# Kernel tuning notes

Measured on AMD Instinct MI355X. Metric: run time of the kernel, lower is better.

## Reference

```python
import jax, jax.numpy as jnp
import numpy as np

NUM_HEADS = 32
HEAD_DIM = 64
ROPE_THETA = 10000.0


def _rope_cos_sin(position_ids, head_dim, theta):
    # inv_freq: [head_dim/2]
    half = head_dim // 2
    inv_freq = 1.0 / (theta ** (jnp.arange(0, half, dtype=jnp.float32) * 2.0 / head_dim))
    angles = position_ids.astype(jnp.float32)[..., None] * inv_freq  # [B,S,half]
    return jnp.cos(angles), jnp.sin(angles)


def _apply_rope(x, cos, sin):
    # x: [B,S,H,hd]; cos/sin: [B,S,half] -> broadcast over heads (rotate-half, Llama style)
    half = x.shape[-1] // 2
    x1, x2 = x[..., :half], x[..., half:]
    c = cos[:, :, None, :]
    s = sin[:, :, None, :]
    return jnp.concatenate([x1 * c - x2 * s, x2 * c + x1 * s], axis=-1)


def setup_inputs() -> dict:
    key = jax.random.key(0)
    ks = jax.random.split(key, 8)
    B, S, D = 2, 2048, 2048
    hidden_states = jax.random.normal(ks[0], (B, S, D), dtype=jnp.float32)
    # causal additive mask (is_causal=False in IpexSDP; mask carries causality)
    causal = jnp.tril(jnp.ones((S, S), dtype=jnp.bool_))
    attention_mask = jnp.where(causal, 0.0, -1e9).astype(jnp.float32)[None, None, :, :]
    attention_mask = jnp.broadcast_to(attention_mask, (B, 1, S, S))
    position_ids = jnp.broadcast_to(jnp.arange(S, dtype=jnp.int64)[None, :], (B, S))
    scale = 0.02
    qkv_w = jax.random.normal(ks[1], (3, D, D), dtype=jnp.float32) * scale
    qkv_b = jax.random.normal(ks[2], (3, D), dtype=jnp.float32) * scale
    o_w = jax.random.normal(ks[3], (D, D), dtype=jnp.float32) * scale
    o_b = jax.random.normal(ks[4], (D,), dtype=jnp.float32) * scale
    residual = jax.random.normal(ks[5], (B, S, D), dtype=jnp.float32)
    return {
        'hidden_states': hidden_states,
        'attention_mask': attention_mask,
        'position_ids': position_ids,
        'qkv_w': qkv_w,
        'qkv_b': qkv_b,
        'o_w': o_w,
        'o_b': o_b,
        'residual': residual,
    }


def reference(hidden_states, attention_mask, position_ids, qkv_w, qkv_b, o_w, o_b, residual):
    B, S, D = hidden_states.shape
    H, hd = NUM_HEADS, HEAD_DIM
    # fused QKV projection (weights stored transposed: x @ W), matching mm_qkv_out
    qkv = jnp.einsum('bsd,tde->tbse', hidden_states, qkv_w) + qkv_b[:, None, None, :]
    q = qkv[0].reshape(B, S, H, hd)
    k = qkv[1].reshape(B, S, H, hd)
    v = qkv[2].reshape(B, S, H, hd)
    cos, sin = _rope_cos_sin(position_ids, hd, ROPE_THETA)
    q = _apply_rope(q, cos, sin)
    k = _apply_rope(k, cos, sin)
    scale = 1.0 / jnp.sqrt(jnp.asarray(hd, dtype=hidden_states.dtype))
    # [B,H,S,S]
    scores = jnp.einsum('bqhd,bkhd->bhqk', q, k) * scale + attention_mask
    probs = jax.nn.softmax(scores, axis=-1)
    attn = jnp.einsum('bhqk,bkhd->bqhd', probs, v).reshape(B, S, D)
    # o-proj fused with bias + residual add (matmul_add_add)
    out = attn @ o_w + o_b + residual
    return out
```

## Files before the change

kernel.cpp:

```cpp
#include <hip/hip_runtime.h>
#include <stdint.h>
#include <stdio.h>

#define D_MODEL 2048
#define SEQ     2048
#define NHEADS  32
#define HDIM    64
#define BATCH   2
#define BH      (BATCH * NHEADS)
#define GK      2048

typedef unsigned short u16;
typedef unsigned int   u32;
typedef __attribute__((ext_vector_type(8))) short short8;
typedef __attribute__((ext_vector_type(4))) short s16x4;
typedef __attribute__((ext_vector_type(4))) float f32x4;
typedef __attribute__((ext_vector_type(4))) u32   u32x4;
typedef __attribute__((ext_vector_type(2))) u32   u32x2;

__device__ __forceinline__ float bf2f(u16 x) {
  union { u32 u; float f; } c; c.u = ((u32)x) << 16; return c.f;
}
__device__ __forceinline__ u16 f2bf(float f) {
  union { float f; u32 u; } c; c.f = f;
  u32 u = c.u;
  return (u16)((u + 0x7FFFu + ((u >> 16) & 1u)) >> 16);
}
__device__ __forceinline__ u32 fbits(float f) {
  union { float f; u32 u; } c; c.f = f; return c.u;
}

typedef const __attribute__((address_space(1))) u32* gas_t;
typedef __attribute__((address_space(3))) u32* las_t;
__device__ __forceinline__ void gll16(const void* g, void* l) {
  __builtin_amdgcn_global_load_lds((gas_t)g, (las_t)l, 16, 0, 0);
}

__device__ __forceinline__ void swiz_mn(int pid, int nx, int& mtile, int& ntile) {
  int chunk = 8 * nx;
  int grp = pid / chunk, loc = pid - grp * chunk;
  mtile = grp * 8 + (loc & 7);
  ntile = loc >> 3;
}

__global__ __launch_bounds__(256) void cvt_k(const float* __restrict__ in,
                                             u16* __restrict__ out) {
  int id = blockIdx.x * 256 + threadIdx.x;
  f32x4 v = *(const f32x4*)&in[(size_t)id * 4];
  alignas(8) u16 o[4];
#pragma unroll
  for (int j = 0; j < 4; j++) o[j] = f2bf(v[j]);
  *(u32x2*)&out[(size_t)id * 4] = *(const u32x2*)o;
}

__global__ __launch_bounds__(256) void transpose_cvt_k(const float* __restrict__ qkv_w,
                                                       const float* __restrict__ o_w,
                                                       u16* __restrict__ outT) {
  __shared__ u16 tile[64][72];
  const int z = blockIdx.z;
  const float* inz = (z < 3) ? qkv_w + (size_t)z * D_MODEL * D_MODEL : o_w;
  u16* outz = outT + (size_t)z * D_MODEL * D_MODEL;
  const int r0 = blockIdx.y * 64, c0 = blockIdx.x * 64;
  const int t = threadIdx.x;
  const int lrow = t >> 4, lcol4 = (t & 15) * 4;
#pragma unroll
  for (int i = 0; i < 4; i++) {
    int r = lrow + i * 16;
    f32x4 v = *(const f32x4*)&inz[(size_t)(r0 + r) * D_MODEL + (c0 + lcol4)];
#pragma unroll
    for (int j = 0; j < 4; j++) tile[r][lcol4 + j] = f2bf(v[j]);
  }
  __syncthreads();
  const int row = t >> 3, col8 = (t & 7) * 8;
#pragma unroll
  for (int i = 0; i < 2; i++) {
    int r = row + i * 32;
    alignas(16) u16 vals[8];
#pragma unroll
    for (int j = 0; j < 8; j++) vals[j] = tile[col8 + j][r];
    *(u32x4*)&outz[(size_t)(c0 + r) * D_MODEL + (r0 + col8)] = *(const u32x4*)vals;
  }
}

__device__ __forceinline__ void gemm128(const u16* __restrict__ A, const u16* __restrict__ BT,
                                        int m0, int n0, u16* As, u16* Bs, f32x4 acc[4][4]) {
  const int t = threadIdx.x;
  const int lane = t & 63, w = t >> 6;
  const int quad = lane >> 4, l16 = lane & 15;
  const int wr = w >> 1, wc = w & 1;
  const int ldr = lane >> 2, ldc = (lane & 3) * 8;
#pragma unroll
  for (int mt = 0; mt < 4; mt++)
#pragma unroll
    for (int nt = 0; nt < 4; nt++)
#pragma unroll
      for (int i = 0; i < 4; i++) acc[mt][nt][i] = 0.0f;

  for (int k0 = 0; k0 < GK; k0 += 32) {
    __syncthreads();
#pragma unroll
    for (int i = 0; i < 2; i++) {
      int rbase = w * 32 + i * 16;
      gll16(&A[(size_t)(m0 + rbase + ldr) * GK + k0 + ldc], &As[rbase * 32]);
      gll16(&BT[(size_t)(n0 + rbase + ldr) * GK + k0 + ldc], &Bs[rbase * 32]);
    }
    __syncthreads();
    short8 af[4], bf[4];
#pragma unroll
    for (int mt = 0; mt < 4; mt++)
      af[mt] = *(const short8*)&As[(wr * 64 + mt * 16 + l16) * 32 + quad * 8];
#pragma unroll
    for (int nt = 0; nt < 4; nt++)
      bf[nt] = *(const short8*)&Bs[(wc * 64 + nt * 16 + l16) * 32 + quad * 8];
#pragma unroll
    for (int mt = 0; mt < 4; mt++)
#pragma unroll
      for (int nt = 0; nt < 4; nt++)
        acc[mt][nt] = __builtin_amdgcn_mfma_f32_16x16x32_bf16(af[mt], bf[nt], acc[mt][nt], 0, 0, 0);
  }
}


__device__ __forceinline__ short8 lds_frag(const u16* tile, int row, int kh, int quad) {
  int off = row * 128 + ((kh * 64 + quad * 16) ^ ((row & 7) << 4));
  return *(const short8*)((const char*)tile + off);
}

__device__ __forceinline__ void stage_half(const u16* __restrict__ src, int rowbase, int k0,
                                           u16* tile, int h, int w, int srl, int scol) {
  u16* ldsb = tile + h * (128 * 64);
  const u16* g0 = &src[(size_t)(rowbase + h * 128 + srl) * GK + k0 + scol];
  const u16* g1 = &src[(size_t)(rowbase + h * 128 + srl + 8) * GK + k0 + scol];
  gll16(g0, (char*)ldsb + w * 2048);
  gll16(g1, (char*)ldsb + w * 2048 + 1024);
}

__global__ __launch_bounds__(512, 1) void qkv_gemm256_k(const u16* __restrict__ A,
                                                        const u16* __restrict__ BT,
                                                        const float* __restrict__ bias,
                                                        u16* __restrict__ Qb, u16* __restrict__ Kb,
                                                        u16* __restrict__ Vbt) {
  __shared__ u16 As[2][256 * 64];
  __shared__ u16 Bs[2][256 * 64];
  const int t = threadIdx.x, w = t >> 6, lane = t & 63;
  const int quad = lane >> 4, l16 = lane & 15;
  const int wr = w >> 2, wc = w & 3;
  int mtile, ntile;
  swiz_mn(blockIdx.x, 24, mtile, ntile);
  const int m0 = mtile * 256, n0 = ntile * 256;
  const int srl = w * 16 + (lane >> 3);
  const int scol = (((lane & 7) ^ (lane >> 3)) << 3);

  f32x4 acc[8][4];
#pragma unroll
  for (int mf = 0; mf < 8; mf++)
#pragma unroll
    for (int nf = 0; nf < 4; nf++)
#pragma unroll
      for (int i = 0; i < 4; i++) acc[mf][nf][i] = 0.0f;

  const int NT = GK / 64;
  stage_half(A, m0, 0, As[0], 0, w, srl, scol);
  stage_half(A, m0, 0, As[0], 1, w, srl, scol);
  stage_half(BT, n0, 0, Bs[0], 0, w, srl, scol);
  stage_half(BT, n0, 0, Bs[0], 1, w, srl, scol);
  stage_half(A, m0, 64, As[1], 0, w, srl, scol);
  stage_half(A, m0, 64, As[1], 1, w, srl, scol);
  asm volatile("s_waitcnt vmcnt(4)" ::: "memory");
  __builtin_amdgcn_s_barrier();

  for (int kt = 0; kt < NT; kt++) {
    const int cur = kt & 1;
    const u16* Ac = As[cur];
    const u16* Bc = Bs[cur];
    short8 af[8][2], bf[4][2];
#pragma unroll
    for (int mf = 0; mf < 4; mf++) {
      af[mf][0] = lds_frag(Ac, wr * 128 + mf * 16 + l16, 0, quad);
      af[mf][1] = lds_frag(Ac, wr * 128 + mf * 16 + l16, 1, quad);
    }
#pragma unroll
    for (int nf = 0; nf < 2; nf++) {
      bf[nf][0] = lds_frag(Bc, wc * 64 + nf * 16 + l16, 0, quad);
      bf[nf][1] = lds_frag(Bc, wc * 64 + nf * 16 + l16, 1, quad);
    }
    if (kt + 1 < NT) stage_half(BT, n0, (kt + 1) * 64, Bs[cur ^ 1], 0, w, srl, scol);
    __builtin_amdgcn_s_barrier();
    __builtin_amdgcn_s_setprio(1);
#pragma unroll
    for (int mf = 0; mf < 4; mf++)
#pragma unroll
      for (int nf = 0; nf < 2; nf++) {
        acc[mf][nf] = __builtin_amdgcn_mfma_f32_16x16x32_bf16(af[mf][0], bf[nf][0], acc[mf][nf], 0, 0, 0);
        acc[mf][nf] = __builtin_amdgcn_mfma_f32_16x16x32_bf16(af[mf][1], bf[nf][1], acc[mf][nf], 0, 0, 0);
      }
    __builtin_amdgcn_s_setprio(0);
    __builtin_amdgcn_s_barrier();
#pragma unroll
    for (int mf = 4; mf < 8; mf++) {
      af[mf][0] = lds_frag(Ac, wr * 128 + mf * 16 + l16, 0, quad);
      af[mf][1] = lds_frag(Ac, wr * 128 + mf * 16 + l16, 1, quad);
    }
#pragma unroll
    for (int nf = 2; nf < 4; nf++) {
      bf[nf][0] = lds_frag(Bc, wc * 64 + nf * 16 + l16, 0, quad);
      bf[nf][1] = lds_frag(Bc, wc * 64 + nf * 16 + l16, 1, quad);
    }
    if (kt + 1 < NT) stage_half(BT, n0, (kt + 1) * 64, Bs[cur ^ 1], 1, w, srl, scol);
    __builtin_amdgcn_s_barrier();
    __builtin_amdgcn_s_setprio(1);
#pragma unroll
    for (int mf = 4; mf < 8; mf++)
#pragma unroll
      for (int nf = 0; nf < 2; nf++) {
        acc[mf][nf] = __builtin_amdgcn_mfma_f32_16x16x32_bf16(af[mf][0], bf[nf][0], acc[mf][nf], 0, 0, 0);
        acc[mf][nf] = __builtin_amdgcn_mfma_f32_16x16x32_bf16(af[mf][1], bf[nf][1], acc[mf][nf], 0, 0, 0);
      }
    __builtin_amdgcn_s_setprio(0);
    __builtin_amdgcn_s_barrier();
    if (kt + 2 < NT) stage_half(A, m0, (kt + 2) * 64, As[cur], 0, w, srl, scol);
    __builtin_amdgcn_s_barrier();
    __builtin_amdgcn_s_setprio(1);
#pragma unroll
    for (int mf = 0; mf < 4; mf++)
#pragma unroll
      for (int nf = 2; nf < 4; nf++) {
        acc[mf][nf] = __builtin_amdgcn_mfma_f32_16x16x32_bf16(af[mf][0], bf[nf][0], acc[mf][nf], 0, 0, 0);
        acc[mf][nf] = __builtin_amdgcn_mfma_f32_16x16x32_bf16(af[mf][1], bf[nf][1], acc[mf][nf], 0, 0, 0);
      }
    __builtin_amdgcn_s_setprio(0);
    __builtin_amdgcn_s_barrier();
    if (kt + 2 < NT) stage_half(A, m0, (kt + 2) * 64, As[cur], 1, w, srl, scol);
    __builtin_amdgcn_s_barrier();
    __builtin_amdgcn_s_setprio(1);
#pragma unroll
    for (int mf = 4; mf < 8; mf++)
#pragma unroll
      for (int nf = 2; nf < 4; nf++) {
        acc[mf][nf] = __builtin_amdgcn_mfma_f32_16x16x32_bf16(af[mf][0], bf[nf][0], acc[mf][nf], 0, 0, 0);
        acc[mf][nf] = __builtin_amdgcn_mfma_f32_16x16x32_bf16(af[mf][1], bf[nf][1], acc[mf][nf], 0, 0, 0);
      }
    __builtin_amdgcn_s_setprio(0);
    if (kt + 2 < NT) {
      asm volatile("s_waitcnt vmcnt(4)" ::: "memory");
    } else {
      asm volatile("s_waitcnt vmcnt(0)" ::: "memory");
    }
    __builtin_amdgcn_s_barrier();
  }

  const int tsel = n0 >> 11;
  if (tsel < 2) {
    u16* dst = tsel ? Kb : Qb;
#pragma unroll
    for (int p = 0; p < 2; p++) {
      int nlo = n0 + wc * 64 + p * 16 + l16;
      float blo = bias[nlo], bhi = bias[nlo + 32];
      int j = p * 16 + l16;
      float inv = __expf((float)j * -0.28782313662425572f);
      int h = (nlo & 2047) >> 6;
#pragma unroll
      for (int mf = 0; mf < 8; mf++) {
#pragma unroll
        for (int r = 0; r < 4; r++) {
          int m = m0 + wr * 128 + mf * 16 + quad * 4 + r;
          int b = m >> 11, s = m & (SEQ - 1);
          float sn, cs;
          __sincosf((float)s * inv, &sn, &cs);
          float x1 = acc[mf][p][r] + blo;
          float x2 = acc[mf][p + 2][r] + bhi;
          size_t base = ((size_t)((b * NHEADS + h) * SEQ + s)) * HDIM;
          dst[base + j]      = f2bf(x1 * cs - x2 * sn);
          dst[base + j + 32] = f2bf(x2 * cs + x1 * sn);
        }
      }
    }
  } else {
#pragma unroll
    for (int nf = 0; nf < 4; nf++) {
      int n = n0 + wc * 64 + nf * 16 + l16;
      float bv = bias[n];
      int e = n & 2047, h = e >> 6, d = e & 63;
#pragma unroll
      for (int mf = 0; mf < 8; mf++) {
        int m0r = m0 + wr * 128 + mf * 16 + quad * 4;
        int b = m0r >> 11, s0 = m0r & (SEQ - 1);
        alignas(8) u16 o4[4];
#pragma unroll
        for (int r = 0; r < 4; r++) o4[r] = f2bf(acc[mf][nf][r] + bv);
        *(u32x2*)&Vbt[((size_t)((b * NHEADS + h) * HDIM + d)) * SEQ + s0] = *(const u32x2*)o4;
      }
    }
  }
}

__global__ __launch_bounds__(256) void oproj_gemm_k(const u16* __restrict__ A, const u16* __restrict__ BT,
                                                    const float* __restrict__ bias,
                                                    const float* __restrict__ resid,
                                                    float* __restrict__ out) {
  __shared__ u16 As[128 * 32], Bs[128 * 32];
  f32x4 acc[4][4];
  int mtile, ntile;
  swiz_mn(blockIdx.x, 16, mtile, ntile);
  const int m0 = mtile * 128, n0 = ntile * 128;
  gemm128(A, BT, m0, n0, As, Bs, acc);
  const int t = threadIdx.x, lane = t & 63, quad = lane >> 4, l16 = lane & 15;
  const int w = t >> 6, wr = w >> 1, wc = w & 1;
#pragma unroll
  for (int nt = 0; nt < 4; nt++) {
    int n = n0 + wc * 64 + nt * 16 + l16;
    float bv = bias[n];
#pragma unroll
    for (int mt = 0; mt < 4; mt++) {
#pragma unroll
      for (int r = 0; r < 4; r++) {
        int m = m0 + wr * 64 + mt * 16 + quad * 4 + r;
        size_t oi = (size_t)m * D_MODEL + n;
        out[oi] = acc[mt][nt][r] + bv + resid[oi];
      }
    }
  }
}

__global__ __launch_bounds__(256, 2) void attn_k(const u16* __restrict__ Qb,
                                                 const u16* __restrict__ Kb,
                                                 const u16* __restrict__ Vbt,
                                                 u16* __restrict__ attn) {
  __shared__ u16 smem[128 * 72];
  u16* Ks = smem;
  u16* Vt = smem + 64 * 72;
  const int blk = blockIdx.x;
  const int bh = blk & 63, pi = blk >> 6;
  const int b = bh >> 5, h = bh & 31;
  const int t = threadIdx.x, w = t >> 6, lane = t & 63, quad = lane >> 4, l16 = lane & 15;
  const int qbT[2] = { pi * 128, (15 - pi) * 128 };
  const int qwT[2] = { qbT[0] + w * 32, qbT[1] + w * 32 };
  const size_t bho = (size_t)bh * SEQ * HDIM;
  const size_t vbo = (size_t)bh * HDIM * SEQ;
  const int kend = qbT[1] + 128;

  short8 qf[2][2][2];
#pragma unroll
  for (int Ti = 0; Ti < 2; Ti++)
#pragma unroll
    for (int qt = 0; qt < 2; qt++)
#pragma unroll
      for (int kd = 0; kd < 2; kd++) {
        short8 v = *(const short8*)&Qb[bho + (size_t)(qwT[Ti] + qt * 16 + l16) * HDIM + kd * 32 + quad * 8];
#pragma unroll
        for (int i = 0; i < 8; i++) {
          float f = bf2f((u16)v[i]) * 0.125f;
          v[i] = (short)f2bf(f);
        }
        qf[Ti][qt][kd] = v;
      }

  f32x4 Oacc[2][4][2];
  float mrow[2][2] = {{-1e30f, -1e30f}, {-1e30f, -1e30f}};
  float lrow[2][2] = {{0.0f, 0.0f}, {0.0f, 0.0f}};
#pragma unroll
  for (int Ti = 0; Ti < 2; Ti++)
#pragma unroll
    for (int dt = 0; dt < 4; dt++)
#pragma unroll
      for (int qt = 0; qt < 2; qt++)
#pragma unroll
        for (int i = 0; i < 4; i++) Oacc[Ti][dt][qt][i] = 0.0f;

  const int srow = t >> 3, sc8 = (t & 7) * 8;
  u32x4 kreg[2], vreg[2];

#pragma unroll
  for (int j = 0; j < 2; j++) {
    kreg[j] = *(const u32x4*)&Kb[bho + (size_t)(srow + j * 32) * HDIM + sc8];
    vreg[j] = *(const u32x4*)&Vbt[vbo + (size_t)(srow + j * 32) * SEQ + sc8];
  }
#pragma unroll
  for (int j = 0; j < 2; j++) {
    *(u32x4*)&Ks[(srow + j * 32) * 72 + sc8] = kreg[j];
    *(u32x4*)&Vt[(srow + j * 32) * 72 + sc8] = vreg[j];
  }
  __syncthreads();

  for (int key0 = 0; key0 < kend; key0 += 64) {
    const int nxt = key0 + 64;
    if (nxt < kend) {
#pragma unroll
      for (int j = 0; j < 2; j++) {
        kreg[j] = *(const u32x4*)&Kb[bho + (size_t)(nxt + srow + j * 32) * HDIM + sc8];
        vreg[j] = *(const u32x4*)&Vbt[vbo + (size_t)(srow + j * 32) * SEQ + nxt + sc8];
      }
    }
#pragma unroll
    for (int Ti = 0; Ti < 2; Ti++) {
      const int qw = qwT[Ti];
      if (key0 <= qw + 31) {
        const int lim = qw + 31 - key0;
        int nkt = (lim >> 4) + 1; if (nkt > 4) nkt = 4;
        f32x4 sacc[4][2];
#pragma unroll
        for (int kt = 0; kt < 4; kt++) {
          if (kt < nkt) {
            short8 kf0 = *(const short8*)&Ks[(kt * 16 + l16) * 72 + quad * 8];
            short8 kf1 = *(const short8*)&Ks[(kt * 16 + l16) * 72 + 32 + quad * 8];
#pragma unroll
            for (int qt = 0; qt < 2; qt++) {
              f32x4 z = {0.0f, 0.0f, 0.0f, 0.0f};
              z = __builtin_amdgcn_mfma_f32_16x16x32_bf16(kf0, qf[Ti][qt][0], z, 0, 0, 0);
              z = __builtin_amdgcn_mfma_f32_16x16x32_bf16(kf1, qf[Ti][qt][1], z, 0, 0, 0);
              sacc[kt][qt] = z;
            }
          }
        }
        if (key0 + 63 > qw) {
#pragma unroll
          for (int qt = 0; qt < 2; qt++) {
            int qrow = qw + qt * 16 + l16;
#pragma unroll
            for (int kt = 0; kt < 4; kt++)
              if (kt < nkt)
#pragma unroll
                for (int r = 0; r < 4; r++)
                  if (key0 + kt * 16 + quad * 4 + r > qrow) sacc[kt][qt][r] = -1e30f;
          }
        }
        float alpha[2];
#pragma unroll
        for (int qt = 0; qt < 2; qt++) {
          float mx = -1e30f;
#pragma unroll
          for (int kt = 0; kt < 4; kt++)
            if (kt < nkt)
#pragma unroll
              for (int r = 0; r < 4; r++) mx = fmaxf(mx, sacc[kt][qt][r]);
          mx = fmaxf(mx, __shfl_xor(mx, 16));
          mx = fmaxf(mx, __shfl_xor(mx, 32));
          float mnew = fmaxf(mrow[Ti][qt], mx);
          alpha[qt] = __expf(mrow[Ti][qt] - mnew);
          mrow[Ti][qt] = mnew;
          float rsum = 0.0f;
#pragma unroll
          for (int kt = 0; kt < 4; kt++)
            if (kt < nkt)
#pragma unroll
              for (int r = 0; r < 4; r++) {
                float pv = __expf(sacc[kt][qt][r] - mnew);
                sacc[kt][qt][r] = pv;
                rsum += pv;
              }
          rsum += __shfl_xor(rsum, 16);
          rsum += __shfl_xor(rsum, 32);
          lrow[Ti][qt] = lrow[Ti][qt] * alpha[qt] + rsum;
        }
#pragma unroll
        for (int dt = 0; dt < 4; dt++)
#pragma unroll
          for (int qt = 0; qt < 2; qt++)
#pragma unroll
            for (int r = 0; r < 4; r++) Oacc[Ti][dt][qt][r] *= alpha[qt];
#pragma unroll
        for (int kt = 0; kt < 4; kt++) {
          if (kt < nkt) {
            s16x4 pk[2];
#pragma unroll
            for (int qt = 0; qt < 2; qt++) {
              u32 a0 = fbits(sacc[kt][qt][0]) + 0x8000u;
              u32 a1 = fbits(sacc[kt][qt][1]) + 0x8000u;
              u32 a2 = fbits(sacc[kt][qt][2]) + 0x8000u;
              u32 a3 = fbits(sacc[kt][qt][3]) + 0x8000u;
              union { u32 u[2]; s16x4 s; } pc;
              pc.u[0] = __builtin_amdgcn_perm(a1, a0, 0x07060302u);
              pc.u[1] = __builtin_amdgcn_perm(a3, a2, 0x07060302u);
              pk[qt] = pc.s;
            }
            s16x4 vf[4];
#pragma unroll
            for (int dt = 0; dt < 4; dt++)
              vf[dt] = *(const s16x4*)&Vt[(dt * 16 + l16) * 72 + kt * 16 + quad * 4];
#pragma unroll
            for (int dt = 0; dt < 4; dt++)
#pragma unroll
              for (int qt = 0; qt < 2; qt++)
                Oacc[Ti][dt][qt] = __builtin_amdgcn_mfma_f32_16x16x16bf16_1k(vf[dt], pk[qt], Oacc[Ti][dt][qt], 0, 0, 0);
          }
        }
      }
    }
    __syncthreads();
    if (nxt < kend) {
#pragma unroll
      for (int j = 0; j < 2; j++) {
        *(u32x4*)&Ks[(srow + j * 32) * 72 + sc8] = kreg[j];
        *(u32x4*)&Vt[(srow + j * 32) * 72 + sc8] = vreg[j];
      }
      __syncthreads();
    }
  }

#pragma unroll
  for (int Ti = 0; Ti < 2; Ti++) {
    float invl[2] = {1.0f / lrow[Ti][0], 1.0f / lrow[Ti][1]};
#pragma unroll
    for (int dt = 0; dt < 4; dt++)
#pragma unroll
      for (int qt = 0; qt < 2; qt++)
#pragma unroll
        for (int r = 0; r < 4; r++)
          smem[(w * 32 + qt * 16 + l16) * 72 + dt * 16 + quad * 4 + r] =
              f2bf(Oacc[Ti][dt][qt][r] * invl[qt]);
    __syncthreads();
#pragma unroll
    for (int ii = 0; ii < 4; ii++) {
      int chunk = t + ii * 256;
      int row = chunk >> 3, g = chunk & 7;
      *(u32x4*)&attn[((size_t)(b * SEQ + qbT[Ti] + row)) * D_MODEL + h * 64 + g * 8] =
          *(const u32x4*)&smem[row * 72 + g * 8];
    }
    __syncthreads();
  }
}

extern "C" void kernel_launch(void* const* d_in, const int* in_sizes, int n_in,
                              void* d_out, int out_size, void* d_ws, size_t ws_size,
                              hipStream_t stream) {
  (void)in_sizes; (void)n_in; (void)out_size;
  const float* hidden = (const float*)d_in[0];
  const float* qkv_w = (const float*)d_in[3];
  const float* qkv_b = (const float*)d_in[4];
  const float* o_w   = (const float*)d_in[5];
  const float* o_b   = (const float*)d_in[6];
  const float* resid = (const float*)d_in[7];
  float* out = (float*)d_out;

  u16* ws = (u16*)d_ws;
  size_t off = 0;
  u16* hidb  = ws + off; off += (size_t)BATCH * SEQ * D_MODEL;
  u16* qkvT  = ws + off; off += (size_t)3 * D_MODEL * D_MODEL;
  u16* owT   = ws + off; off += (size_t)D_MODEL * D_MODEL;
  u16* Qb    = ws + off; off += (size_t)BH * SEQ * HDIM;
  u16* Kb    = ws + off; off += (size_t)BH * SEQ * HDIM;
  u16* Vbt   = ws + off; off += (size_t)BH * SEQ * HDIM;
  u16* attnb = ws + off; off += (size_t)BATCH * SEQ * D_MODEL;
  if (ws_size < off * sizeof(u16)) {
    fprintf(stderr, "kernel_launch: workspace too small: need %zu bytes, have %zu\n",
            off * sizeof(u16), ws_size);
    return;
  }
  (void)owT;

  cvt_k<<<(BATCH * SEQ * D_MODEL) / (4 * 256), 256, 0, stream>>>(hidden, hidb);
  transpose_cvt_k<<<dim3(32, 32, 4), 256, 0, stream>>>(qkv_w, o_w, qkvT);
  qkv_gemm256_k<<<16 * 24, 512, 0, stream>>>(hidb, qkvT, qkv_b, Qb, Kb, Vbt);
  attn_k<<<BH * 8, 256, 0, stream>>>(Qb, Kb, Vbt, attnb);
  oproj_gemm_k<<<16 * 32, 256, 0, stream>>>(attnb, owT, o_b, resid, out);
}
```

Before: 428.8 us.

## Hand-schedule QKV GEMM LDS fragment reads with inline asm and explicit fences

Replaces compiler-generated LDS fragment loads in the QKV GEMM main loop with inline ds_read_b128 on precomputed LDS addresses and swizzle offsets. Explicit lgkmcnt(0) waits and sched_barriers pin the instruction schedule. The B fragments for the second column half move to just before the phase that uses them, which spreads LDS reads across the four MFMA phases. Removing the memory clobbers lets the compiler keep values in registers, but correctness now rests on the hand-placed waits.

```diff
diff --git a/kernel.cpp b/kernel.cpp
--- a/kernel.cpp
+++ b/kernel.cpp
@@ -34,6 +34,14 @@
 typedef __attribute__((address_space(3))) u32* las_t;
 __device__ __forceinline__ void gll16(const void* g, void* l) {
   __builtin_amdgcn_global_load_lds((gas_t)g, (las_t)l, 16, 0, 0);
+}
+__device__ __forceinline__ u32 lds_addr(const void* p) {
+  return (u32)(size_t)(const __attribute__((address_space(3))) void*)p;
+}
+__device__ __forceinline__ short8 ds_read128(u32 addr) {
+  short8 r;
+  asm volatile("ds_read_b128 %0, %1" : "=v"(r) : "v"(addr));
+  return r;
 }
 
 __device__ __forceinline__ void swiz_mn(int pid, int nx, int& mtile, int& ntile) {
@@ -121,11 +129,6 @@
 }
 
 
-__device__ __forceinline__ short8 lds_frag(const u16* tile, int row, int kh, int quad) {
-  int off = row * 128 + ((kh * 64 + quad * 16) ^ ((row & 7) << 4));
-  return *(const short8*)((const char*)tile + off);
-}
-
 __device__ __forceinline__ void stage_half(const u16* __restrict__ src, int rowbase, int k0,
                                            u16* tile, int h, int w, int srl, int scol) {
   u16* ldsb = tile + h * (128 * 64);
@@ -134,6 +137,8 @@
   gll16(g0, (char*)ldsb + w * 2048);
   gll16(g1, (char*)ldsb + w * 2048 + 1024);
 }
+
+#define LGKM0_FENCE  do { asm volatile("s_waitcnt lgkmcnt(0)"); __builtin_amdgcn_sched_barrier(0); } while (0)
 
 __global__ __launch_bounds__(512, 1) void qkv_gemm256_k(const u16* __restrict__ A,
                                                         const u16* __restrict__ BT,
@@ -151,6 +156,12 @@
   const int srl = w * 16 + (lane >> 3);
   const int scol = (((lane & 7) ^ (lane >> 3)) << 3);
 
+  const u32 asb0 = lds_addr(As[0]), asb1 = lds_addr(As[1]);
+  const u32 bsb0 = lds_addr(Bs[0]), bsb1 = lds_addr(Bs[1]);
+  const u32 xorc = (u32)((l16 & 7) << 4);
+  const u32 cq0 = (u32)(quad * 16) ^ xorc;
+  const u32 cq1 = (u32)(64 + quad * 16) ^ xorc;
+
   f32x4 acc[8][4];
 #pragma unroll
   for (int mf = 0; mf < 8; mf++)
@@ -166,26 +177,32 @@
   stage_half(BT, n0, 0, Bs[0], 1, w, srl, scol);
   stage_half(A, m0, 64, As[1], 0, w, srl, scol);
   stage_half(A, m0, 64, As[1], 1, w, srl, scol);
-  asm volatile("s_waitcnt vmcnt(4)" ::: "memory");
+  asm volatile("s_waitcnt vmcnt(4)");
+  __builtin_amdgcn_sched_barrier(0);
   __builtin_amdgcn_s_barrier();
 
   for (int kt = 0; kt < NT; kt++) {
     const int cur = kt & 1;
-    const u16* Ac = As[cur];
-    const u16* Bc = Bs[cur];
+    const u32 aA = cur ? asb1 : asb0;
+    const u32 aB = cur ? bsb1 : bsb0;
+    u16* Acur = cur ? (u16*)As[1] : (u16*)As[0];
+    u16* Bnxt = cur ? (u16*)Bs[0] : (u16*)Bs[1];
     short8 af[8][2], bf[4][2];
 #pragma unroll
     for (int mf = 0; mf < 4; mf++) {
-      af[mf][0] = lds_frag(Ac, wr * 128 + mf * 16 + l16, 0, quad);
-      af[mf][1] = lds_frag(Ac, wr * 128 + mf * 16 + l16, 1, quad);
+      u32 rb = aA + (u32)((wr * 128 + mf * 16 + l16) * 128);
+      af[mf][0] = ds_read128(rb + cq0);
+      af[mf][1] = ds_read128(rb + cq1);
     }
 #pragma unroll
     for (int nf = 0; nf < 2; nf++) {
-      bf[nf][0] = lds_frag(Bc, wc * 64 + nf * 16 + l16, 0, quad);
-      bf[nf][1] = lds_frag(Bc, wc * 64 + nf * 16 + l16, 1, quad);
-    }
-    if (kt + 1 < NT) stage_half(BT, n0, (kt + 1) * 64, Bs[cur ^ 1], 0, w, srl, scol);
-    __builtin_amdgcn_s_barrier();
+      u32 rb = aB + (u32)((wc * 64 + nf * 16 + l16) * 128);
+      bf[nf][0] = ds_read128(rb + cq0);
+      bf[nf][1] = ds_read128(rb + cq1);
+    }
+    if (kt + 1 < NT) stage_half(BT, n0, (kt + 1) * 64, Bnxt, 0, w, srl, scol);
+    __builtin_amdgcn_s_barrier();
+    LGKM0_FENCE;
     __builtin_amdgcn_s_setprio(1);
 #pragma unroll
     for (int mf = 0; mf < 4; mf++)
@@ -196,18 +213,16 @@
       }
     __builtin_amdgcn_s_setprio(0);
     __builtin_amdgcn_s_barrier();
+    __builtin_amdgcn_sched_barrier(0);
 #pragma unroll
     for (int mf = 4; mf < 8; mf++) {
-      af[mf][0] = lds_frag(Ac, wr * 128 + mf * 16 + l16, 0, quad);
-      af[mf][1] = lds_frag(Ac, wr * 128 + mf * 16 + l16, 1, quad);
-    }
-#pragma unroll
-    for (int nf = 2; nf < 4; nf++) {
-      bf[nf][0] = lds_frag(Bc, wc * 64 + nf * 16 + l16, 0, quad);
-      bf[nf][1] = lds_frag(Bc, wc * 64 + nf * 16 + l16, 1, quad);
-    }
-    if (kt + 1 < NT) stage_half(BT, n0, (kt + 1) * 64, Bs[cur ^ 1], 1, w, srl, scol);
-    __builtin_amdgcn_s_barrier();
+      u32 rb = aA + (u32)((wr * 128 + mf * 16 + l16) * 128);
+      af[mf][0] = ds_read128(rb + cq0);
+      af[mf][1] = ds_read128(rb + cq1);
+    }
+    if (kt + 1 < NT) stage_half(BT, n0, (kt + 1) * 64, Bnxt, 1, w, srl, scol);
+    __builtin_amdgcn_s_barrier();
+    LGKM0_FENCE;
     __builtin_amdgcn_s_setprio(1);
 #pragma unroll
     for (int mf = 4; mf < 8; mf++)
@@ -218,8 +233,16 @@
       }
     __builtin_amdgcn_s_setprio(0);
     __builtin_amdgcn_s_barrier();
-    if (kt + 2 < NT) stage_half(A, m0, (kt + 2) * 64, As[cur], 0, w, srl, scol);
-    __builtin_amdgcn_s_barrier();
+    __builtin_amdgcn_sched_barrier(0);
+#pragma unroll
+    for (int nf = 2; nf < 4; nf++) {
+      u32 rb = aB + (u32)((wc * 64 + nf * 16 + l16) * 128);
+      bf[nf][0] = ds_read128(rb + cq0);
+      bf[nf][1] = ds_read128(rb + cq1);
+    }
+    if (kt + 2 < NT) stage_half(A, m0, (kt + 2) * 64, Acur, 0, w, srl, scol);
+    __builtin_amdgcn_s_barrier();
+    LGKM0_FENCE;
     __builtin_amdgcn_s_setprio(1);
 #pragma unroll
     for (int mf = 0; mf < 4; mf++)
@@ -230,7 +253,8 @@
       }
     __builtin_amdgcn_s_setprio(0);
     __builtin_amdgcn_s_barrier();
-    if (kt + 2 < NT) stage_half(A, m0, (kt + 2) * 64, As[cur], 1, w, srl, scol);
+    __builtin_amdgcn_sched_barrier(0);
+    if (kt + 2 < NT) stage_half(A, m0, (kt + 2) * 64, Acur, 1, w, srl, scol);
     __builtin_amdgcn_s_barrier();
     __builtin_amdgcn_s_setprio(1);
 #pragma unroll
@@ -242,11 +266,13 @@
       }
     __builtin_amdgcn_s_setprio(0);
     if (kt + 2 < NT) {
-      asm volatile("s_waitcnt vmcnt(4)" ::: "memory");
+      asm volatile("s_waitcnt vmcnt(4)");
     } else {
-      asm volatile("s_waitcnt vmcnt(0)" ::: "memory");
-    }
-    __builtin_amdgcn_s_barrier();
+      asm volatile("s_waitcnt vmcnt(0)");
+    }
+    __builtin_amdgcn_sched_barrier(0);
+    __builtin_amdgcn_s_barrier();
+    __builtin_amdgcn_sched_barrier(0);
   }
 
   const int tsel = n0 >> 11;
```

After: 426.1 us. No clear change (-0.6%).
